# Performance work log

Measured on AMD Instinct MI355X. Metric: run time of the kernel, lower is better.

The kernel has to match this reference:

```python
import jax, jax.numpy as jnp
import numpy as np

N_NODES = 100000
N_EDGES = 3200000
IN_DIM = 512
HID_DIM = 16


def spmm(edge_src, edge_dst, edge_weight, feats):
    # out[i] = sum_{(j->i) in E} w_e * feats[j]  (sparse adj @ feats)
    gathered = feats[edge_src] * edge_weight[:, None]  # [E, D]
    return jax.ops.segment_sum(gathered, edge_dst, num_segments=N_NODES)


def setup_inputs() -> dict:
    key = jax.random.key(0)
    ks = jax.random.split(key, 8)
    x = jax.random.normal(ks[0], (N_NODES, IN_DIM), dtype=jnp.float32)
    edge_src = jax.random.randint(ks[1], (N_EDGES,), 0, N_NODES, dtype=jnp.int32)
    edge_dst = jax.random.randint(ks[2], (N_EDGES,), 0, N_NODES, dtype=jnp.int32)
    # normalized adjacency weights (positive, small, like D^-1/2 A D^-1/2 entries)
    edge_weight = jax.random.uniform(ks[3], (N_EDGES,), dtype=jnp.float32) * 0.1
    # Glorot-style init for GraphConvolution weights
    W1 = jax.random.normal(ks[4], (IN_DIM, HID_DIM), dtype=jnp.float32) * (1.0 / np.sqrt(IN_DIM))
    b1 = jnp.zeros((HID_DIM,), dtype=jnp.float32)
    W2 = jax.random.normal(ks[5], (HID_DIM, 1), dtype=jnp.float32) * (1.0 / np.sqrt(HID_DIM))
    b2 = jnp.zeros((1,), dtype=jnp.float32)
    return {"x": x, "edge_src": edge_src, "edge_dst": edge_dst,
            "edge_weight": edge_weight, "W1": W1, "b1": b1, "W2": W2, "b2": b2}


def reference(x, edge_src, edge_dst, edge_weight, W1, b1, W2, b2):
    # Layer 1: GraphConvolution(input_dim -> hidden_dim) + ReLU
    h = spmm(edge_src, edge_dst, edge_weight, x @ W1) + b1  # [N, 16]
    h = jax.nn.relu(h)
    # dropout is identity in eval mode (training=False)
    # Layer 2: GraphConvolution(hidden_dim -> 1)
    out = spmm(edge_src, edge_dst, edge_weight, h @ W2) + b2  # [N, 1]
    return out
```

## Files before the change

### kernel.cpp

```cpp
#include <hip/hip_runtime.h>
#include <hip/hip_fp16.h>

#define N_NODES 100000
#define N_EDGES 3200000
#define IN_DIM  512
#define HID_DIM 16

#define B_BKT   782
#define BKT_SH  7
#define EPB     12500
#define CAP_MAX 4608

#define G1_TILES 6250

typedef __attribute__((ext_vector_type(8))) short bf16x8;
typedef __attribute__((ext_vector_type(4))) float f32x4;

__device__ __forceinline__ void atomic_add_f32(float* p, float v) {
    __hip_atomic_fetch_add(p, v, __ATOMIC_RELAXED, __HIP_MEMORY_SCOPE_AGENT);
}
__device__ __forceinline__ int atomic_add_i32(int* p, int v) {
    return __hip_atomic_fetch_add(p, v, __ATOMIC_RELAXED, __HIP_MEMORY_SCOPE_AGENT);
}

__device__ __forceinline__ unsigned short bf16_rne(float f) {
    unsigned u = __float_as_uint(f);
    return (unsigned short)((u + 0x7fffu + ((u >> 16) & 1u)) >> 16);
}

__global__ void z0_init(int* __restrict__ cursor, int cap) {
    int b = blockIdx.x * blockDim.x + threadIdx.x;
    if (b < B_BKT) cursor[b] = b * cap;
}

__global__ __launch_bounds__(256) void g1_xw_mfma(const float* __restrict__ x,
                                                  const float* __restrict__ W1,
                                                  __half* __restrict__ xwh) {
    __shared__ alignas(16) unsigned short whi[16 * 64 * 8];
    __shared__ alignas(16) unsigned short wlo[16 * 64 * 8];
    const int t = threadIdx.x;

    for (int idx = t; idx < 16 * 64 * 8; idx += 256) {
        int c  = idx >> 9;
        int l  = (idx >> 3) & 63;
        int tt = idx & 7;
        int k  = c * 32 + ((l >> 4) << 3) + tt;
        int j  = l & 15;
        float w = W1[k * HID_DIM + j];
        unsigned u = __float_as_uint(w);
        float hif = __uint_as_float(u & 0xffff0000u);
        whi[idx] = (unsigned short)(u >> 16);
        wlo[idx] = bf16_rne(w - hif);
    }
    __syncthreads();

    const int lane = t & 63;
    const int wid  = blockIdx.x * 4 + (t >> 6);
    if (wid >= G1_TILES) return;
    const int row0 = wid * 16;

    const float* xrow = x + (size_t)(row0 + (lane & 15)) * IN_DIM + ((lane >> 4) << 3);
    const unsigned short* whp = &whi[lane * 8];
    const unsigned short* wlp = &wlo[lane * 8];

    f32x4 acc = {0.f, 0.f, 0.f, 0.f};
    float4 p0[2], p1[2];
    p0[0] = *(const float4*)(xrow);
    p1[0] = *(const float4*)(xrow + 4);
    p0[1] = *(const float4*)(xrow + 32);
    p1[1] = *(const float4*)(xrow + 36);
#pragma unroll
    for (int c = 0; c < 16; ++c) {
        const int cur = c & 1;
        float4 n0, n1;
        if (c < 14) {
            n0 = *(const float4*)(xrow + (c + 2) * 32);
            n1 = *(const float4*)(xrow + (c + 2) * 32 + 4);
        }
        float av[8] = {p0[cur].x, p0[cur].y, p0[cur].z, p0[cur].w,
                       p1[cur].x, p1[cur].y, p1[cur].z, p1[cur].w};
        bf16x8 ah, al;
#pragma unroll
        for (int e = 0; e < 8; ++e) {
            unsigned u = __float_as_uint(av[e]);
            ah[e] = (short)(u >> 16);
            float lof = av[e] - __uint_as_float(u & 0xffff0000u);
            al[e] = (short)bf16_rne(lof);
        }
        bf16x8 bh = *(const bf16x8*)(whp + (size_t)c * 512);
        bf16x8 bl = *(const bf16x8*)(wlp + (size_t)c * 512);
        acc = __builtin_amdgcn_mfma_f32_16x16x32_bf16(ah, bh, acc, 0, 0, 0);
        acc = __builtin_amdgcn_mfma_f32_16x16x32_bf16(al, bh, acc, 0, 0, 0);
        acc = __builtin_amdgcn_mfma_f32_16x16x32_bf16(ah, bl, acc, 0, 0, 0);
        if (c < 14) { p0[cur] = n0; p1[cur] = n1; }
    }

    const int n     = lane & 15;
    const int rbase = row0 + ((lane >> 4) << 2);
#pragma unroll
    for (int i = 0; i < 4; ++i)
        xwh[(size_t)(rbase + i) * HID_DIM + n] = __float2half_rn(acc[i]);
}

__global__ __launch_bounds__(1024) void s1_bin(const int* __restrict__ src,
                                               const int* __restrict__ dst,
                                               const float* __restrict__ wgt,
                                               int* __restrict__ cursor,
                                               uint2* __restrict__ rec, int cap) {
    __shared__ int hist[B_BKT];
    __shared__ int base[B_BKT];
    const int t = threadIdx.x;
    for (int b = t; b < B_BKT; b += 1024) hist[b] = 0;
    __syncthreads();
    const int e0 = blockIdx.x * EPB;
    const int4*   d4 = (const int4*)(dst + e0);
    const int4*   s4 = (const int4*)(src + e0);
    const float4* w4 = (const float4*)(wgt + e0);
    const int NG = EPB / 4;
    for (int g = t; g < NG; g += 1024) {
        int4 d = d4[g];
        atomicAdd(&hist[d.x >> BKT_SH], 1);
        atomicAdd(&hist[d.y >> BKT_SH], 1);
        atomicAdd(&hist[d.z >> BKT_SH], 1);
        atomicAdd(&hist[d.w >> BKT_SH], 1);
    }
    __syncthreads();
    for (int b = t; b < B_BKT; b += 1024) {
        int c = hist[b];
        base[b] = c > 0 ? atomic_add_i32(&cursor[b], c) : 0;
    }
    __syncthreads();
    for (int b = t; b < B_BKT; b += 1024) hist[b] = 0;
    __syncthreads();
    for (int g = t; g < NG; g += 1024) {
        int4 d = d4[g];
        int4 s = s4[g];
        float4 w = w4[g];
        {
            int b = d.x >> BKT_SH;
            int pos = base[b] + atomicAdd(&hist[b], 1);
            rec[pos] = make_uint2(((unsigned)s.x << BKT_SH) | (unsigned)(d.x & 127),
                                  __float_as_uint(w.x));
        }
        {
            int b = d.y >> BKT_SH;
            int pos = base[b] + atomicAdd(&hist[b], 1);
            rec[pos] = make_uint2(((unsigned)s.y << BKT_SH) | (unsigned)(d.y & 127),
                                  __float_as_uint(w.y));
        }
        {
            int b = d.z >> BKT_SH;
            int pos = base[b] + atomicAdd(&hist[b], 1);
            rec[pos] = make_uint2(((unsigned)s.z << BKT_SH) | (unsigned)(d.z & 127),
                                  __float_as_uint(w.z));
        }
        {
            int b = d.w >> BKT_SH;
            int pos = base[b] + atomicAdd(&hist[b], 1);
            rec[pos] = make_uint2(((unsigned)s.w << BKT_SH) | (unsigned)(d.w & 127),
                                  __float_as_uint(w.w));
        }
    }
}

__global__ __launch_bounds__(512) void s2p4(const int* __restrict__ cursor,
                                            uint2* __restrict__ rec,
                                            int2* __restrict__ row,
                                            const __half* __restrict__ xwh,
                                            const float* __restrict__ b1,
                                            const float* __restrict__ W2,
                                            float* __restrict__ hw, int cap) {
    __shared__ uint2 srt[CAP_MAX];
    __shared__ int ocnt[128], scn[128], cur[128];
    const int t = threadIdx.x;
    const int bkt = blockIdx.x;
    const int e0 = bkt * cap;
    int n = cursor[bkt] - e0;
    n = max(0, min(n, cap));
    if (t < 128) ocnt[t] = 0;
    __syncthreads();
    for (int i = t; i < n; i += 512)
        atomicAdd(&ocnt[rec[e0 + i].x & 127u], 1);
    __syncthreads();
    if (t < 128) scn[t] = ocnt[t];
    __syncthreads();
    for (int off = 1; off < 128; off <<= 1) {
        int v = 0;
        if (t < 128 && t >= off) v = scn[t - off];
        __syncthreads();
        if (t < 128 && t >= off) scn[t] += v;
        __syncthreads();
    }
    if (t < 128) {
        int b = scn[t] - ocnt[t];
        cur[t] = b;
        int node = (bkt << BKT_SH) + t;
        if (node < N_NODES) row[node] = make_int2(e0 + b, ocnt[t]);
    }
    __syncthreads();
    for (int i = t; i < n; i += 512) {
        uint2 r = rec[e0 + i];
        int d = (int)(r.x & 127u);
        int pos = atomicAdd(&cur[d], 1);
        srt[pos] = make_uint2(r.x >> BKT_SH, r.y);
    }
    __syncthreads();
    for (int i = t; i < n; i += 512) rec[e0 + i] = srt[i];
    const int j = t & 15;
    for (int g = (t >> 4); g < 128; g += 32) {
        const int node = (bkt << BKT_SH) + g;
        if (node >= N_NODES) continue;
        int e = scn[g] - ocnt[g];
        const int end = scn[g];
        float acc = 0.0f;
        for (; e + 4 <= end; e += 4) {
            uint2 q0 = srt[e], q1 = srt[e + 1], q2 = srt[e + 2], q3 = srt[e + 3];
            float f0 = __half2float(xwh[(size_t)q0.x * HID_DIM + j]);
            float f1 = __half2float(xwh[(size_t)q1.x * HID_DIM + j]);
            float f2 = __half2float(xwh[(size_t)q2.x * HID_DIM + j]);
            float f3 = __half2float(xwh[(size_t)q3.x * HID_DIM + j]);
            acc += __uint_as_float(q0.y) * f0;
            acc += __uint_as_float(q1.y) * f1;
            acc += __uint_as_float(q2.y) * f2;
            acc += __uint_as_float(q3.y) * f3;
        }
        for (; e < end; ++e) {
            uint2 q = srt[e];
            acc += __uint_as_float(q.y) * __half2float(xwh[(size_t)q.x * HID_DIM + j]);
        }
        float v = fmaxf(acc + b1[j], 0.0f) * W2[j];
        v += __shfl_xor(v, 1);
        v += __shfl_xor(v, 2);
        v += __shfl_xor(v, 4);
        v += __shfl_xor(v, 8);
        if (j == 0) hw[node] = v;
    }
}

__global__ __launch_bounds__(256) void p5_layer2(const int2* __restrict__ row,
                                                 const uint2* __restrict__ rec,
                                                 const float* __restrict__ hwv,
                                                 const float* __restrict__ b2,
                                                 float* __restrict__ out) {
    const int t = threadIdx.x;
    const int node = blockIdx.x * 32 + (t >> 3);
    const int i = t & 7;
    int2 r = row[node];
    const int end = r.x + r.y;
    int k = r.x + i;
    float s = 0.0f;
    for (; k + 24 < end; k += 32) {
        uint2 a = rec[k], b = rec[k + 8], c = rec[k + 16], d = rec[k + 24];
        float ha = hwv[a.x], hb = hwv[b.x], hc = hwv[c.x], hd = hwv[d.x];
        s += __uint_as_float(a.y) * ha + __uint_as_float(b.y) * hb
           + __uint_as_float(c.y) * hc + __uint_as_float(d.y) * hd;
    }
    for (; k < end; k += 8) {
        uint2 a = rec[k];
        s += __uint_as_float(a.y) * hwv[a.x];
    }
    s += __shfl_xor(s, 1);
    s += __shfl_xor(s, 2);
    s += __shfl_xor(s, 4);
    if (i == 0) out[node] = b2[0] + s;
}

__global__ void f0_zero(float* __restrict__ h, const float* __restrict__ b2,
                        float* __restrict__ out) {
    int i = blockIdx.x * blockDim.x + threadIdx.x;
    if (i < N_NODES * HID_DIM) h[i] = 0.0f;
    if (i < N_NODES) out[i] = b2[0];
}
__global__ void k2_spmm1(const int* __restrict__ src, const int* __restrict__ dst,
                         const float* __restrict__ wgt, const __half* __restrict__ xwh,
                         float* __restrict__ h) {
    int t = blockIdx.x * blockDim.x + threadIdx.x;
    int e = t >> 4;
    int j = t & (HID_DIM - 1);
    if (e < N_EDGES) {
        float v = wgt[e] * __half2float(xwh[(size_t)src[e] * HID_DIM + j]);
        atomic_add_f32(&h[(size_t)dst[e] * HID_DIM + j], v);
    }
}
__global__ void k3_act(const float* __restrict__ h, const float* __restrict__ b1,
                       const float* __restrict__ W2, float* __restrict__ hw) {
    int i = blockIdx.x * blockDim.x + threadIdx.x;
    if (i >= N_NODES) return;
    const float4* h4 = (const float4*)(h + (size_t)i * HID_DIM);
    const float4* b4 = (const float4*)b1;
    const float4* w4 = (const float4*)W2;
    float acc = 0.0f;
#pragma unroll
    for (int q = 0; q < HID_DIM / 4; ++q) {
        float4 hv = h4[q]; float4 bv = b4[q]; float4 wv = w4[q];
        acc += fmaxf(hv.x + bv.x, 0.0f) * wv.x;
        acc += fmaxf(hv.y + bv.y, 0.0f) * wv.y;
        acc += fmaxf(hv.z + bv.z, 0.0f) * wv.z;
        acc += fmaxf(hv.w + bv.w, 0.0f) * wv.w;
    }
    hw[i] = acc;
}
__global__ void k4_spmm2(const int* __restrict__ src, const int* __restrict__ dst,
                         const float* __restrict__ wgt, const float* __restrict__ hw,
                         float* __restrict__ out) {
    int e = blockIdx.x * blockDim.x + threadIdx.x;
    if (e < N_EDGES) atomic_add_f32(&out[dst[e]], wgt[e] * hw[src[e]]);
}


extern "C" void kernel_launch(void* const* d_in, const int* in_sizes, int n_in,
                              void* d_out, int out_size, void* d_ws, size_t ws_size,
                              hipStream_t stream) {
    const float* x    = (const float*)d_in[0];
    const int*   esrc = (const int*)  d_in[1];
    const int*   edst = (const int*)  d_in[2];
    const float* ew   = (const float*)d_in[3];
    const float* W1   = (const float*)d_in[4];
    const float* b1   = (const float*)d_in[5];
    const float* W2   = (const float*)d_in[6];
    const float* b2   = (const float*)d_in[7];
    float* out = (float*)d_out;
    char* ws = (char*)d_ws;

    __half* xwh    = (__half*)ws;
    float*  hw     = (float*)(ws + (size_t)N_NODES * HID_DIM * 2);
    int*    cursor = (int*)(hw + N_NODES);
    int2*   row    = (int2*)(((size_t)(cursor + B_BKT) + 7) & ~(size_t)7);
    size_t rec_off = ((size_t)((char*)(row + N_NODES) - ws) + 15) & ~(size_t)15;
    uint2* rec = (uint2*)(ws + rec_off);

    int cap = 0;
    if (ws_size > rec_off) {
        size_t cap_fit = (ws_size - rec_off) / ((size_t)B_BKT * sizeof(uint2));
        cap = (int)(cap_fit < CAP_MAX ? cap_fit : CAP_MAX);
    }

    if (cap >= 4480) {
        z0_init<<<(B_BKT + 255) / 256, 256, 0, stream>>>(cursor, cap);
        g1_xw_mfma<<<(G1_TILES + 3) / 4, 256, 0, stream>>>(x, W1, xwh);
        s1_bin<<<N_EDGES / EPB, 1024, 0, stream>>>(esrc, edst, ew, cursor, rec, cap);
        s2p4<<<B_BKT, 512, 0, stream>>>(cursor, rec, row, xwh, b1, W2, hw, cap);
        p5_layer2<<<N_NODES / 32, 256, 0, stream>>>(row, rec, hw, b2, out);
    } else {
        __half* f_xwh = (__half*)ws;
        float*  f_h   = (float*)(ws + (size_t)N_NODES * HID_DIM * 2);
        float*  f_hw  = f_h + (size_t)N_NODES * HID_DIM;
        int n = N_NODES * HID_DIM;
        f0_zero<<<(n + 255) / 256, 256, 0, stream>>>(f_h, b2, out);
        g1_xw_mfma<<<(G1_TILES + 3) / 4, 256, 0, stream>>>(x, W1, f_xwh);
        k2_spmm1<<<(N_EDGES * 16) / 256, 256, 0, stream>>>(esrc, edst, ew, f_xwh, f_h);
        k3_act<<<(N_NODES + 255) / 256, 256, 0, stream>>>(f_h, b1, W2, f_hw);
        k4_spmm2<<<(N_EDGES + 255) / 256, 256, 0, stream>>>(esrc, edst, ew, f_hw, out);
    }
}
```

Before: 418.4 us.

## Stage binned edge records in LDS before coalesced global scatter

The binning kernel now counting-sorts each block's edges by bucket in shared memory, using a local prefix scan, and then writes them to global memory. Consecutive threads write consecutive records within each bucket run, replacing fully random 8-byte global stores. Blocks shrink from 12500 to 5000 edges, so there are more blocks and more per-bucket cursor atomics. Each block also pays for an extra LDS pass and a scan with many barriers.

```diff
diff --git a/kernel.cpp b/kernel.cpp
--- a/kernel.cpp
+++ b/kernel.cpp
@@ -8,7 +8,8 @@
 
 #define B_BKT   782
 #define BKT_SH  7
-#define EPB     12500
+#define EPB2    5000
+#define NBLK2   640
 #define CAP_MAX 4608
 
 #define G1_TILES 6250
@@ -102,22 +103,28 @@
         xwh[(size_t)(rbase + i) * HID_DIM + n] = __float2half_rn(acc[i]);
 }
 
-__global__ __launch_bounds__(1024) void s1_bin(const int* __restrict__ src,
+__global__ __launch_bounds__(512) void s1_bin2(const int* __restrict__ src,
                                                const int* __restrict__ dst,
                                                const float* __restrict__ wgt,
                                                int* __restrict__ cursor,
                                                uint2* __restrict__ rec, int cap) {
+    __shared__ uint2 srt[EPB2];
+    __shared__ unsigned short bkt[EPB2];
     __shared__ int hist[B_BKT];
-    __shared__ int base[B_BKT];
+    __shared__ int lbase[B_BKT];
+    __shared__ int gbase[B_BKT];
+    __shared__ int scn[512];
     const int t = threadIdx.x;
-    for (int b = t; b < B_BKT; b += 1024) hist[b] = 0;
-    __syncthreads();
-    const int e0 = blockIdx.x * EPB;
+    for (int b = t; b < B_BKT; b += 512) hist[b] = 0;
+    __syncthreads();
+
+    const int e0 = blockIdx.x * EPB2;
     const int4*   d4 = (const int4*)(dst + e0);
     const int4*   s4 = (const int4*)(src + e0);
     const float4* w4 = (const float4*)(wgt + e0);
-    const int NG = EPB / 4;
-    for (int g = t; g < NG; g += 1024) {
+    const int NG = EPB2 / 4;
+
+    for (int g = t; g < NG; g += 512) {
         int4 d = d4[g];
         atomicAdd(&hist[d.x >> BKT_SH], 1);
         atomicAdd(&hist[d.y >> BKT_SH], 1);
@@ -125,41 +132,71 @@
         atomicAdd(&hist[d.w >> BKT_SH], 1);
     }
     __syncthreads();
-    for (int b = t; b < B_BKT; b += 1024) {
+
+    int c0 = 0, c1 = 0;
+    if (t < 391) { c0 = hist[2 * t]; c1 = hist[2 * t + 1]; }
+    int s = c0 + c1;
+    scn[t] = s;
+    __syncthreads();
+    for (int off = 1; off < 512; off <<= 1) {
+        int v = (t >= off) ? scn[t - off] : 0;
+        __syncthreads();
+        scn[t] += v;
+        __syncthreads();
+    }
+    int excl = scn[t] - s;
+    if (t < 391) {
+        lbase[2 * t]     = excl;
+        lbase[2 * t + 1] = excl + c0;
+    }
+    __syncthreads();
+
+    for (int b = t; b < B_BKT; b += 512) {
         int c = hist[b];
-        base[b] = c > 0 ? atomic_add_i32(&cursor[b], c) : 0;
-    }
-    __syncthreads();
-    for (int b = t; b < B_BKT; b += 1024) hist[b] = 0;
-    __syncthreads();
-    for (int g = t; g < NG; g += 1024) {
+        gbase[b] = c > 0 ? atomic_add_i32(&cursor[b], c) : 0;
+    }
+    __syncthreads();
+    for (int b = t; b < B_BKT; b += 512) hist[b] = lbase[b];
+    __syncthreads();
+
+    for (int g = t; g < NG; g += 512) {
         int4 d = d4[g];
-        int4 s = s4[g];
+        int4 sv = s4[g];
         float4 w = w4[g];
         {
             int b = d.x >> BKT_SH;
-            int pos = base[b] + atomicAdd(&hist[b], 1);
-            rec[pos] = make_uint2(((unsigned)s.x << BKT_SH) | (unsigned)(d.x & 127),
+            int pos = atomicAdd(&hist[b], 1);
+            srt[pos] = make_uint2(((unsigned)sv.x << BKT_SH) | (unsigned)(d.x & 127),
                                   __float_as_uint(w.x));
+            bkt[pos] = (unsigned short)b;
         }
         {
             int b = d.y >> BKT_SH;
-            int pos = base[b] + atomicAdd(&hist[b], 1);
-            rec[pos] = make_uint2(((unsigned)s.y << BKT_SH) | (unsigned)(d.y & 127),
+            int pos = atomicAdd(&hist[b], 1);
+            srt[pos] = make_uint2(((unsigned)sv.y << BKT_SH) | (unsigned)(d.y & 127),
                                   __float_as_uint(w.y));
+            bkt[pos] = (unsigned short)b;
         }
         {
             int b = d.z >> BKT_SH;
-            int pos = base[b] + atomicAdd(&hist[b], 1);
-            rec[pos] = make_uint2(((unsigned)s.z << BKT_SH) | (unsigned)(d.z & 127),
+            int pos = atomicAdd(&hist[b], 1);
+            srt[pos] = make_uint2(((unsigned)sv.z << BKT_SH) | (unsigned)(d.z & 127),
                                   __float_as_uint(w.z));
+            bkt[pos] = (unsigned short)b;
         }
         {
             int b = d.w >> BKT_SH;
-            int pos = base[b] + atomicAdd(&hist[b], 1);
-            rec[pos] = make_uint2(((unsigned)s.w << BKT_SH) | (unsigned)(d.w & 127),
+            int pos = atomicAdd(&hist[b], 1);
+            srt[pos] = make_uint2(((unsigned)sv.w << BKT_SH) | (unsigned)(d.w & 127),
                                   __float_as_uint(w.w));
-        }
+            bkt[pos] = (unsigned short)b;
+        }
+    }
+    __syncthreads();
+
+    for (int i = t; i < EPB2; i += 512) {
+        int b = bkt[i];
+        rec[gbase[b] + (i - lbase[b])] = srt[i];
     }
 }
 
@@ -338,7 +375,7 @@
     if (cap >= 4480) {
         z0_init<<<(B_BKT + 255) / 256, 256, 0, stream>>>(cursor, cap);
         g1_xw_mfma<<<(G1_TILES + 3) / 4, 256, 0, stream>>>(x, W1, xwh);
-        s1_bin<<<N_EDGES / EPB, 1024, 0, stream>>>(esrc, edst, ew, cursor, rec, cap);
+        s1_bin2<<<NBLK2, 512, 0, stream>>>(esrc, edst, ew, cursor, rec, cap);
         s2p4<<<B_BKT, 512, 0, stream>>>(cursor, rec, row, xwh, b1, W2, hw, cap);
         p5_layer2<<<N_NODES / 32, 256, 0, stream>>>(row, rec, hw, b2, out);
     } else {
```

Result: faster. 406.6 us (-2.8%).
